# Optimization experiments

Hardware: AMD Instinct MI355X
Metric: run time of the kernel (lower is better)

## Reference

```python
import jax, jax.numpy as jnp
import numpy as np

RADIUS = 3
T_STEPS = 2
NEG = -9.0e8
B, L, DEG = 256, 64, 6
FEAT, BOND, FP, OUT = 39, 10, 256, 1


def _leaky(x):
    return jax.nn.leaky_relu(x, 0.01)


def _gru(x, h, wih, whh, bih, bhh):
    # PyTorch GRUCell: gates ordered (r, z, n)
    gi = x @ wih.T + bih
    gh = h @ whh.T + bhh
    ir, iz, inn = jnp.split(gi, 3, axis=-1)
    hr, hz, hn = jnp.split(gh, 3, axis=-1)
    r = jax.nn.sigmoid(ir + hr)
    z = jax.nn.sigmoid(iz + hz)
    n = jnp.tanh(inn + r * hn)
    return (1.0 - z) * n + z * h


def _forward(atom_list, bond_list, atom_mask,
             atom_fc_w, atom_fc_b, neighbor_fc_w, neighbor_fc_b,
             align_w, align_b, attend_w, attend_b,
             gru_wih, gru_whh, gru_bih, gru_bhh,
             mol_align_w, mol_align_b, mol_attend_w, mol_attend_b,
             mol_gru_wih, mol_gru_whh, mol_gru_bih, mol_gru_bhh,
             out_w, out_b,
             atom_degree_list, bond_degree_list):
    b, l, _ = atom_list.shape
    mask = atom_mask[..., None]                                   # [B,L,1]
    atom_feature = _leaky(atom_list @ atom_fc_w.T + atom_fc_b)    # [B,L,FP]

    # per-molecule neighbor gather (padding index = L-1)
    bidx = jnp.arange(b)[:, None, None]
    atom_nb = atom_list[bidx, atom_degree_list]                    # [B,L,deg,FEAT]
    bond_nb = bond_list[bidx, bond_degree_list]                    # [B,L,deg,BOND]
    neighbor_feature = _leaky(
        jnp.concatenate([atom_nb, bond_nb], axis=-1) @ neighbor_fc_w.T + neighbor_fc_b
    )                                                              # [B,L,deg,FP]

    attend_mask = (atom_degree_list != l - 1).astype(atom_feature.dtype)[..., None]
    softmax_mask = jnp.where(atom_degree_list == l - 1, NEG, 0.0).astype(atom_feature.dtype)[..., None]

    for d in range(RADIUS):
        af_exp = jnp.broadcast_to(atom_feature[:, :, None, :], neighbor_feature.shape)
        feature_align = jnp.concatenate([af_exp, neighbor_feature], axis=-1)  # [B,L,deg,2FP]
        align_score = _leaky(feature_align @ align_w[d].T + align_b[d]) + softmax_mask
        attention_weight = jax.nn.softmax(align_score, axis=-2) * attend_mask
        attended = neighbor_feature @ attend_w[d].T + attend_b[d]
        context = jax.nn.elu(jnp.sum(attention_weight * attended, axis=-2))   # [B,L,FP]
        atom_feature = _gru(context.reshape(b * l, -1), atom_feature.reshape(b * l, -1),
                            gru_wih[d], gru_whh[d], gru_bih[d], gru_bhh[d]).reshape(b, l, -1)
        # faithful to original: self-feature broadcast across neighbor dim
        neighbor_feature = jnp.broadcast_to(jax.nn.relu(atom_feature)[:, :, None, :],
                                            neighbor_feature.shape)

    mol_feature = jnp.sum(jax.nn.relu(atom_feature) * mask, axis=-2)          # [B,FP]
    mol_softmax_mask = jnp.where(atom_mask == 0, NEG, 0.0).astype(atom_feature.dtype)[..., None]

    for _ in range(T_STEPS):
        m_exp = jnp.broadcast_to(mol_feature[:, None, :], atom_feature.shape)
        mol_align = jnp.concatenate([m_exp, atom_feature], axis=-1)           # [B,L,2FP]
        mol_score = _leaky(mol_align @ mol_align_w.T + mol_align_b) + mol_softmax_mask
        mol_w = jax.nn.softmax(mol_score, axis=-2) * mask
        attended = atom_feature @ mol_attend_w.T + mol_attend_b
        mol_context = jax.nn.elu(jnp.sum(mol_w * attended, axis=-2))
        mol_feature = _gru(mol_context, mol_feature,
                           mol_gru_wih, mol_gru_whh, mol_gru_bih, mol_gru_bhh)

    mol_prediction = mol_feature @ out_w.T + out_b
    return atom_feature, mol_prediction


def setup_inputs() -> dict:
    key = jax.random.key(0)
    ks = jax.random.split(key, 20)
    s = 0.05
    return {
        "atom_list": jax.random.normal(ks[0], (B, L, FEAT), jnp.float32),
        "bond_list": jax.random.normal(ks[1], (B, L, BOND), jnp.float32),
        "atom_degree_list": jax.random.randint(ks[2], (B, L, DEG), 0, L),
        "bond_degree_list": jax.random.randint(ks[3], (B, L, DEG), 0, L),
        "atom_mask": jnp.ones((B, L), jnp.float32),
        "atom_fc_w": jax.random.normal(ks[4], (FP, FEAT)) * s,
        "atom_fc_b": jnp.zeros((FP,)),
        "neighbor_fc_w": jax.random.normal(ks[5], (FP, FEAT + BOND)) * s,
        "neighbor_fc_b": jnp.zeros((FP,)),
        "align_w": jax.random.normal(ks[6], (RADIUS, 1, 2 * FP)) * s,
        "align_b": jnp.zeros((RADIUS, 1)),
        "attend_w": jax.random.normal(ks[7], (RADIUS, FP, FP)) * s,
        "attend_b": jnp.zeros((RADIUS, FP)),
        "gru_wih": jax.random.normal(ks[8], (RADIUS, 3 * FP, FP)) * s,
        "gru_whh": jax.random.normal(ks[9], (RADIUS, 3 * FP, FP)) * s,
        "gru_bih": jnp.zeros((RADIUS, 3 * FP)),
        "gru_bhh": jnp.zeros((RADIUS, 3 * FP)),
        "mol_align_w": jax.random.normal(ks[10], (1, 2 * FP)) * s,
        "mol_align_b": jnp.zeros((1,)),
        "mol_attend_w": jax.random.normal(ks[11], (FP, FP)) * s,
        "mol_attend_b": jnp.zeros((FP,)),
        "mol_gru_wih": jax.random.normal(ks[12], (3 * FP, FP)) * s,
        "mol_gru_whh": jax.random.normal(ks[13], (3 * FP, FP)) * s,
        "mol_gru_bih": jnp.zeros((3 * FP,)),
        "mol_gru_bhh": jnp.zeros((3 * FP,)),
        "out_w": jax.random.normal(ks[14], (OUT, FP)) * s,
        "out_b": jnp.zeros((OUT,)),
    }


def reference(atom_list, bond_list, atom_degree_list, bond_degree_list, atom_mask,
              atom_fc_w, atom_fc_b, neighbor_fc_w, neighbor_fc_b,
              align_w, align_b, attend_w, attend_b,
              gru_wih, gru_whh, gru_bih, gru_bhh,
              mol_align_w, mol_align_b, mol_attend_w, mol_attend_b,
              mol_gru_wih, mol_gru_whh, mol_gru_bih, mol_gru_bhh,
              out_w, out_b):
    return _forward(atom_list, bond_list, atom_mask,
                    atom_fc_w, atom_fc_b, neighbor_fc_w, neighbor_fc_b,
                    align_w, align_b, attend_w, attend_b,
                    gru_wih, gru_whh, gru_bih, gru_bhh,
                    mol_align_w, mol_align_b, mol_attend_w, mol_attend_b,
                    mol_gru_wih, mol_gru_whh, mol_gru_bih, mol_gru_bhh,
                    out_w, out_b,
                    atom_degree_list, bond_degree_list)
```

## Files before the change

kernel.cpp:

```cpp
#include <hip/hip_runtime.h>
#include <hip/hip_bf16.h>

#define NB 256
#define NL 64
#define DEG 6
#define FEAT 39
#define BOND 10
#define FP 256
#define NEGV (-9.0e8f)

using s16x8 = __attribute__((ext_vector_type(8))) short;
using f32x4 = __attribute__((ext_vector_type(4))) float;

__device__ __forceinline__ unsigned short f2bf(float f){
  unsigned u = __float_as_uint(f);
  u += 0x7fffu + ((u >> 16) & 1u);
  return (unsigned short)(u >> 16);
}
__device__ __forceinline__ float lo16(unsigned u){ return __uint_as_float(u << 16); }
__device__ __forceinline__ float hi16(unsigned u){ return __uint_as_float(u & 0xffff0000u); }

__device__ __forceinline__ float block_sum256(float v, float* scr){
  #pragma unroll
  for(int o=32;o>0;o>>=1) v += __shfl_down(v, o, 64);
  __syncthreads();
  if((threadIdx.x & 63) == 0) scr[threadIdx.x >> 6] = v;
  __syncthreads();
  return scr[0] + scr[1] + scr[2] + scr[3];
}
__device__ __forceinline__ float wave_allsum(float v){
  #pragma unroll
  for(int o=1;o<64;o<<=1) v += __shfl_xor(v, o, 64);
  return v;
}

#define CVT_N0 196608
#define CVT_N1 589824
#define CVT_N2 589824
#define CVT_N3 65536
#define CVT_N4 196608
#define CVT_N5 196608
#define CVT_TOT (CVT_N0+CVT_N1+CVT_N2+CVT_N3+CVT_N4+CVT_N5)

__global__ void k_cvt_all(const float* __restrict__ a0, const float* __restrict__ a1,
                          const float* __restrict__ a2, const float* __restrict__ a3,
                          const float* __restrict__ a4, const float* __restrict__ a5,
                          unsigned short* __restrict__ dst){
  int i = blockIdx.x*256 + threadIdx.x;
  int off = i; const float* src;
  if(off < CVT_N0) src = a0;
  else { off -= CVT_N0;
    if(off < CVT_N1) src = a1;
    else { off -= CVT_N1;
      if(off < CVT_N2) src = a2;
      else { off -= CVT_N2;
        if(off < CVT_N3) src = a3;
        else { off -= CVT_N3;
          if(off < CVT_N4) src = a4;
          else { off -= CVT_N4; src = a5; } } } } }
  dst[i] = f2bf(src[off]);
}

__global__ void k_tr(const float* __restrict__ aw, const float* __restrict__ nw,
                     float* __restrict__ afcT, unsigned short* __restrict__ nfcT){
  int i = blockIdx.x*256 + threadIdx.x;
  if(i < 40*256){
    int k = i >> 8, r = i & 255;
    afcT[i] = (k < FEAT) ? aw[r*FEAT + k] : 0.f;
  } else {
    int j = i - 40*256;
    int k = j >> 8, r = j & 255;
    nfcT[j] = (k < FEAT+BOND) ? f2bf(nw[r*(FEAT+BOND) + k]) : (unsigned short)0;
  }
}

__global__ __launch_bounds__(256) void k_atom4(const float* __restrict__ atom,
    const float* __restrict__ afcT, const float* __restrict__ bias, float* __restrict__ af){
  __shared__ float WT[40*256];
  __shared__ float x_s[4][40];
  const int t = threadIdx.x, bl0 = blockIdx.x*4;
  for(int v=t; v<2560; v+=256) *(float4*)&WT[v*4] = *(const float4*)&afcT[v*4];
  for(int idx=t; idx<4*FEAT; idx+=256){ int a=idx/FEAT, k=idx%FEAT; x_s[a][k]=atom[(bl0+a)*FEAT+k]; }
  if(t < 4) x_s[t][39] = 0.f;
  __syncthreads();
  const int w = t>>6, t0 = (t&63)*4, row = bl0 + w;
  float4 b4 = *(const float4*)&bias[t0];
  float acc[4] = {b4.x, b4.y, b4.z, b4.w};
  for(int k=0;k<40;++k){
    float iv = x_s[w][k];
    float4 wv = *(const float4*)&WT[(k<<8)+t0];
    acc[0]=fmaf(iv,wv.x,acc[0]); acc[1]=fmaf(iv,wv.y,acc[1]);
    acc[2]=fmaf(iv,wv.z,acc[2]); acc[3]=fmaf(iv,wv.w,acc[3]);
  }
  float4 o;
  o.x = acc[0]>0.f?acc[0]:0.01f*acc[0]; o.y = acc[1]>0.f?acc[1]:0.01f*acc[1];
  o.z = acc[2]>0.f?acc[2]:0.01f*acc[2]; o.w = acc[3]>0.f?acc[3]:0.01f*acc[3];
  *(float4*)&af[(size_t)row*FP + t0] = o;
}

__global__ __launch_bounds__(256) void k_nbr4(const float* __restrict__ atom,
    const float* __restrict__ bond, const int* __restrict__ adl, const int* __restrict__ bdl,
    const unsigned short* __restrict__ nfcT, const float* __restrict__ bn,
    const float* __restrict__ alw, const float* __restrict__ alb,
    const float* __restrict__ af, float* __restrict__ wnf, float* __restrict__ swb){
  __shared__ unsigned short WnT[52*256];
  __shared__ float in_s[4][DEG][52];
  __shared__ int   ai_s[4][DEG];
  const int t = threadIdx.x, bl0 = blockIdx.x*4;
  if(t < 24){ int a=t/6, d=t%6; ai_s[a][d] = adl[(bl0+a)*DEG + d]; }
  for(int v=t; v<1664; v+=256) *(s16x8*)&WnT[v*8] = *(const s16x8*)&nfcT[v*8];
  __syncthreads();
  for(int idx=t; idx<4*DEG*(FEAT+BOND); idx+=256){
    int a = idx/(DEG*(FEAT+BOND)), rem = idx%(DEG*(FEAT+BOND));
    int d = rem/(FEAT+BOND), k = rem%(FEAT+BOND);
    int bb = (bl0+a) >> 6;
    float v;
    if(k < FEAT) v = atom[((size_t)bb*NL + ai_s[a][d])*FEAT + k];
    else { int bi = bdl[(bl0+a)*DEG + d]; v = bond[((size_t)bb*NL + bi)*BOND + (k-FEAT)]; }
    in_s[a][d][k] = v;
  }
  if(t < 24){ int a=t/6, d=t%6; in_s[a][d][49]=0.f; in_s[a][d][50]=0.f; in_s[a][d][51]=0.f; }
  __syncthreads();
  const int w = t>>6, lane = t&63, t0 = lane*4, row = bl0 + w;
  float acc[DEG][4] = {};
  for(int k=0;k<52;++k){
    uint2 u = *(const uint2*)&WnT[(k<<8) + t0];
    float w0=lo16(u.x), w1=hi16(u.x), w2=lo16(u.y), w3=hi16(u.y);
    #pragma unroll
    for(int d=0;d<DEG;++d){
      float iv = in_s[w][d][k];
      acc[d][0]=fmaf(iv,w0,acc[d][0]); acc[d][1]=fmaf(iv,w1,acc[d][1]);
      acc[d][2]=fmaf(iv,w2,acc[d][2]); acc[d][3]=fmaf(iv,w3,acc[d][3]);
    }
  }
  float4 bnv = *(const float4*)&bn[t0];
  float bna[4] = {bnv.x, bnv.y, bnv.z, bnv.w};
  float nf[DEG][4];
  #pragma unroll
  for(int d=0;d<DEG;++d)
    #pragma unroll
    for(int j=0;j<4;++j){ float v = acc[d][j] + bna[j]; nf[d][j] = v>0.f ? v : 0.01f*v; }
  float4 af4 = *(const float4*)&af[(size_t)row*FP + t0];
  float4 a1  = *(const float4*)&alw[t0];
  float4 a2  = *(const float4*)&alw[FP + t0];
  float sa = wave_allsum(af4.x*a1.x + af4.y*a1.y + af4.z*a1.z + af4.w*a1.w);
  float sd[DEG];
  #pragma unroll
  for(int d=0;d<DEG;++d)
    sd[d] = wave_allsum(nf[d][0]*a2.x + nf[d][1]*a2.y + nf[d][2]*a2.z + nf[d][3]*a2.w);
  float ab = alb[0];
  float sc[DEG], msk[DEG];
  #pragma unroll
  for(int d=0;d<DEG;++d){
    float v = sa + sd[d] + ab;
    v = v>0.f ? v : 0.01f*v;
    msk[d] = (ai_s[w][d] == NL-1) ? 0.f : 1.f;
    sc[d] = v + (msk[d] > 0.f ? 0.f : NEGV);
  }
  float m = sc[0];
  #pragma unroll
  for(int d=1;d<DEG;++d) m = fmaxf(m, sc[d]);
  float e[DEG], Z = 0.f;
  #pragma unroll
  for(int d=0;d<DEG;++d){ e[d] = expf(sc[d]-m); Z += e[d]; }
  float wgt[DEG], sw = 0.f;
  #pragma unroll
  for(int d=0;d<DEG;++d){ wgt[d] = e[d]/Z*msk[d]; sw += wgt[d]; }
  float o[4] = {};
  #pragma unroll
  for(int d=0;d<DEG;++d)
    #pragma unroll
    for(int j=0;j<4;++j) o[j] = fmaf(wgt[d], nf[d][j], o[j]);
  float4 ov; ov.x=o[0]; ov.y=o[1]; ov.z=o[2]; ov.w=o[3];
  *(float4*)&wnf[(size_t)row*FP + t0] = ov;
  if(lane == 0) swb[row] = sw;
}

template<int MODE>
__global__ __launch_bounds__(256) void k_ctx_gemm(
    const float* __restrict__ Xsrc, const float* __restrict__ swb,
    const unsigned short* __restrict__ Wbf, const float* __restrict__ bat,
    unsigned short* __restrict__ ctxbf){
  __shared__ unsigned short A_lds[64][264];
  __shared__ unsigned short B_lds[64][264];
  const int t = threadIdx.x;
  const int m0 = (blockIdx.x >> 2) * 64, n0 = (blockIdx.x & 3) * 64;
  const int rb = t >> 4, cb = (t & 15) * 16;
  for(int i=0;i<4;++i){
    int row = i*16 + rb;
    const float* src = Xsrc + (size_t)(m0+row)*FP + cb;
    float mult = MODE ? swb[m0+row] : 1.f;
    unsigned short tmp[16];
    #pragma unroll
    for(int q=0;q<4;++q){
      float4 v = ((const float4*)src)[q];
      if(MODE){ v.x=fmaxf(v.x,0.f)*mult; v.y=fmaxf(v.y,0.f)*mult;
                v.z=fmaxf(v.z,0.f)*mult; v.w=fmaxf(v.w,0.f)*mult; }
      tmp[q*4+0]=f2bf(v.x); tmp[q*4+1]=f2bf(v.y); tmp[q*4+2]=f2bf(v.z); tmp[q*4+3]=f2bf(v.w);
    }
    *(s16x8*)&A_lds[row][cb]   = *(s16x8*)&tmp[0];
    *(s16x8*)&A_lds[row][cb+8] = *(s16x8*)&tmp[8];
    const unsigned short* wsrc = Wbf + (size_t)(n0+row)*FP + cb;
    *(s16x8*)&B_lds[row][cb]   = *(const s16x8*)&wsrc[0];
    *(s16x8*)&B_lds[row][cb+8] = *(const s16x8*)&wsrc[8];
  }
  __syncthreads();
  const int w = t>>6, lane = t&63, lr = lane&15, ks = lane>>4;
  const int wr = (w>>1)*32, wc = (w&1)*32;
  f32x4 acc[2][2] = {};
  #pragma unroll
  for(int kk=0;kk<8;++kk){
    int ko = kk*32 + ks*8;
    s16x8 a0 = *(const s16x8*)&A_lds[wr+lr][ko];
    s16x8 a1 = *(const s16x8*)&A_lds[wr+16+lr][ko];
    s16x8 b0 = *(const s16x8*)&B_lds[wc+lr][ko];
    s16x8 b1 = *(const s16x8*)&B_lds[wc+16+lr][ko];
    acc[0][0] = __builtin_amdgcn_mfma_f32_16x16x32_bf16(a0,b0,acc[0][0],0,0,0);
    acc[0][1] = __builtin_amdgcn_mfma_f32_16x16x32_bf16(a0,b1,acc[0][1],0,0,0);
    acc[1][0] = __builtin_amdgcn_mfma_f32_16x16x32_bf16(a1,b0,acc[1][0],0,0,0);
    acc[1][1] = __builtin_amdgcn_mfma_f32_16x16x32_bf16(a1,b1,acc[1][1],0,0,0);
  }
  #pragma unroll
  for(int fm=0;fm<2;++fm)
    #pragma unroll
    for(int fn=0;fn<2;++fn){
      int n = n0 + wc + fn*16 + lr;
      float batv = bat[n];
      #pragma unroll
      for(int j=0;j<4;++j){
        int m = m0 + wr + fm*16 + ks*4 + j;
        float v = acc[fm][fn][j] + swb[m]*batv;
        v = v > 0.f ? v : expm1f(v);
        ctxbf[(size_t)m*FP + n] = f2bf(v);
      }
    }
}

__global__ __launch_bounds__(256) void k_gates_gru(
    const unsigned short* __restrict__ ctxbf, const float* __restrict__ h_glob,
    const unsigned short* __restrict__ wihbf, const unsigned short* __restrict__ whhbf,
    const float* __restrict__ bih, const float* __restrict__ bhh,
    float* __restrict__ h_out){
  __shared__ unsigned short A_ctx[32][40];
  __shared__ unsigned short A_h[32][40];
  __shared__ unsigned short B_lds[6][64][40];
  const int t = threadIdx.x;
  const int m0 = (blockIdx.x >> 2) * 32, nc = (blockIdx.x & 3) * 64;
  const int w = t>>6, lane = t&63, lr = lane&15, ks = lane>>4;
  const int mh = (w>>1)*16, nh = (w&1)*32;
  f32x4 acc[6][2] = {};
  for(int kk=0;kk<8;++kk){
    const int k0 = kk*32;
    __syncthreads();
    {
      int row = t>>3, c4 = (t&7)*4;
      *(uint2*)&A_ctx[row][c4] = *(const uint2*)(ctxbf + (size_t)(m0+row)*FP + k0 + c4);
      float4 hv = *(const float4*)(h_glob + (size_t)(m0+row)*FP + k0 + c4);
      unsigned short ht[4] = {f2bf(hv.x), f2bf(hv.y), f2bf(hv.z), f2bf(hv.w)};
      *(uint2*)&A_h[row][c4] = *(uint2*)ht;
    }
    #pragma unroll
    for(int i=0;i<6;++i){
      int idx = i*256 + t;
      int s = idx >> 8, rem = idx & 255;
      int row = rem >> 2, c8 = (rem & 3)*8;
      const unsigned short* wsrc = (s < 3)
          ? wihbf + (size_t)(s*FP + nc + row)*FP + k0 + c8
          : whhbf + (size_t)((s-3)*FP + nc + row)*FP + k0 + c8;
      *(s16x8*)&B_lds[s][row][c8] = *(const s16x8*)wsrc;
    }
    __syncthreads();
    s16x8 ac = *(const s16x8*)&A_ctx[mh+lr][ks*8];
    s16x8 ah = *(const s16x8*)&A_h[mh+lr][ks*8];
    #pragma unroll
    for(int s=0;s<6;++s){
      s16x8 a = (s < 3) ? ac : ah;
      #pragma unroll
      for(int fn=0;fn<2;++fn){
        s16x8 b = *(const s16x8*)&B_lds[s][nh+fn*16+lr][ks*8];
        acc[s][fn] = __builtin_amdgcn_mfma_f32_16x16x32_bf16(a,b,acc[s][fn],0,0,0);
      }
    }
  }
  #pragma unroll
  for(int fn=0;fn<2;++fn){
    int n = nc + nh + fn*16 + lr;
    float bir = bih[n], biz = bih[FP+n], bin_ = bih[2*FP+n];
    float bhr = bhh[n], bhz = bhh[FP+n], bhn  = bhh[2*FP+n];
    #pragma unroll
    for(int j=0;j<4;++j){
      int m = m0 + mh + ks*4 + j;
      float h = h_glob[(size_t)m*FP + n];
      float ir = acc[0][fn][j]+bir, iz = acc[1][fn][j]+biz, inn = acc[2][fn][j]+bin_;
      float hr = acc[3][fn][j]+bhr, hz = acc[4][fn][j]+bhz, hn  = acc[5][fn][j]+bhn;
      float r = 1.f/(1.f + expf(-(ir+hr)));
      float z = 1.f/(1.f + expf(-(iz+hz)));
      float ng = tanhf(inn + r*hn);
      h_out[(size_t)m*FP + n] = (1.f-z)*ng + z*h;
    }
  }
}

__global__ __launch_bounds__(256) void k_lin_gemm(
    const float* __restrict__ Xsrc, const unsigned short* __restrict__ Wbf,
    const float* __restrict__ bias, float* __restrict__ Y){
  __shared__ unsigned short A_lds[64][264];
  __shared__ unsigned short B_lds[64][264];
  const int t = threadIdx.x;
  const int m0 = (blockIdx.x >> 2) * 64, n0 = (blockIdx.x & 3) * 64;
  const int rb = t >> 4, cb = (t & 15) * 16;
  for(int i=0;i<4;++i){
    int row = i*16 + rb;
    const float* src = Xsrc + (size_t)(m0+row)*FP + cb;
    unsigned short tmp[16];
    #pragma unroll
    for(int q=0;q<4;++q){
      float4 v = ((const float4*)src)[q];
      tmp[q*4+0]=f2bf(v.x); tmp[q*4+1]=f2bf(v.y); tmp[q*4+2]=f2bf(v.z); tmp[q*4+3]=f2bf(v.w);
    }
    *(s16x8*)&A_lds[row][cb]   = *(s16x8*)&tmp[0];
    *(s16x8*)&A_lds[row][cb+8] = *(s16x8*)&tmp[8];
    const unsigned short* wsrc = Wbf + (size_t)(n0+row)*FP + cb;
    *(s16x8*)&B_lds[row][cb]   = *(const s16x8*)&wsrc[0];
    *(s16x8*)&B_lds[row][cb+8] = *(const s16x8*)&wsrc[8];
  }
  __syncthreads();
  const int w = t>>6, lane = t&63, lr = lane&15, ks = lane>>4;
  const int wr = (w>>1)*32, wc = (w&1)*32;
  f32x4 acc[2][2] = {};
  #pragma unroll
  for(int kk=0;kk<8;++kk){
    int ko = kk*32 + ks*8;
    s16x8 a0 = *(const s16x8*)&A_lds[wr+lr][ko];
    s16x8 a1 = *(const s16x8*)&A_lds[wr+16+lr][ko];
    s16x8 b0 = *(const s16x8*)&B_lds[wc+lr][ko];
    s16x8 b1 = *(const s16x8*)&B_lds[wc+16+lr][ko];
    acc[0][0] = __builtin_amdgcn_mfma_f32_16x16x32_bf16(a0,b0,acc[0][0],0,0,0);
    acc[0][1] = __builtin_amdgcn_mfma_f32_16x16x32_bf16(a0,b1,acc[0][1],0,0,0);
    acc[1][0] = __builtin_amdgcn_mfma_f32_16x16x32_bf16(a1,b0,acc[1][0],0,0,0);
    acc[1][1] = __builtin_amdgcn_mfma_f32_16x16x32_bf16(a1,b1,acc[1][1],0,0,0);
  }
  #pragma unroll
  for(int fm=0;fm<2;++fm)
    #pragma unroll
    for(int fn=0;fn<2;++fn){
      int n = n0 + wc + fn*16 + lr;
      float bv = bias[n];
      #pragma unroll
      for(int j=0;j<4;++j){
        int m = m0 + wr + fm*16 + ks*4 + j;
        Y[(size_t)m*FP + n] = acc[fm][fn][j] + bv;
      }
    }
}

__global__ void k_finalize(const float* __restrict__ af, const float* __restrict__ mask,
                           float* __restrict__ molfeat, float* __restrict__ out_af){
  const int b = blockIdx.x, t = threadIdx.x;
  __shared__ float msk_s[NL];
  if(t < NL) msk_s[t] = mask[b*NL + t];
  __syncthreads();
  float mf = 0.f;
  for(int l=0;l<NL;++l){
    float v = af[(size_t)(b*NL + l)*FP + t];
    out_af[(size_t)(b*NL + l)*FP + t] = v;
    mf = fmaf(fmaxf(v,0.f), msk_s[l], mf);
  }
  molfeat[b*FP + t] = mf;
}

__global__ void k_mol_ctx(const float* __restrict__ af, const float* __restrict__ att,
    const float* __restrict__ mfin, const float* __restrict__ maw,
    const float* __restrict__ mabp, const float* __restrict__ mask,
    unsigned short* __restrict__ ctxb){
  const int b = blockIdx.x, t = threadIdx.x;
  __shared__ float mf_s[FP];
  __shared__ float sc_s[NL], aw_s[NL], scr[4];
  mf_s[t] = mfin[b*FP + t];
  __syncthreads();
  float sa = block_sum256(maw[t]*mf_s[t], scr);
  int l = t >> 2, q = t & 3;
  float p = 0.f;
  {
    const float* ar = af + (size_t)(b*NL + l)*FP + q*64;
    const float* w2 = maw + FP + q*64;
    for(int k=0;k<64;++k) p = fmaf(ar[k], w2[k], p);
  }
  p += __shfl_xor(p, 1, 64);
  p += __shfl_xor(p, 2, 64);
  if(q == 0){
    float mv = mask[b*NL + l];
    float v = sa + p + mabp[0];
    v = v > 0.f ? v : 0.01f*v;
    sc_s[l] = v + (mv == 0.f ? NEGV : 0.f);
  }
  __syncthreads();
  if(t < NL){
    float s = sc_s[t];
    float m = s;
    #pragma unroll
    for(int o=32;o>0;o>>=1) m = fmaxf(m, __shfl_xor(m, o, 64));
    float e = expf(s - m);
    float Z = e;
    #pragma unroll
    for(int o=32;o>0;o>>=1) Z += __shfl_xor(Z, o, 64);
    aw_s[t] = e / Z * mask[b*NL + t];
  }
  __syncthreads();
  float acc = 0.f;
  for(int l2=0;l2<NL;++l2) acc = fmaf(aw_s[l2], att[(size_t)(b*NL + l2)*FP + t], acc);
  float c = acc > 0.f ? acc : expm1f(acc);
  ctxb[b*FP + t] = f2bf(c);
}

__global__ void k_out(const float* __restrict__ molfeat, const float* __restrict__ ow,
                      const float* __restrict__ ob, float* __restrict__ outp){
  const int b = blockIdx.x, t = threadIdx.x;
  __shared__ float scr[4];
  float s = block_sum256(molfeat[b*FP + t]*ow[t], scr);
  if(t == 0) outp[b] = s + ob[0];
}

__global__ void k_atom_fc(const float* __restrict__ atom, const float* __restrict__ W,
                          const float* __restrict__ bias, float* __restrict__ af){
  const int row = blockIdx.x;
  const int t = threadIdx.x;
  __shared__ float x[FEAT];
  if(t < FEAT) x[t] = atom[row*FEAT + t];
  __syncthreads();
  float acc = bias[t];
  const float* wr = W + t*FEAT;
  #pragma unroll
  for(int k=0;k<FEAT;++k) acc = fmaf(x[k], wr[k], acc);
  af[row*FP + t] = acc > 0.f ? acc : 0.01f*acc;
}

__global__ void k_nbr_align(const float* __restrict__ atom, const float* __restrict__ bond,
    const int* __restrict__ adl, const int* __restrict__ bdl,
    const float* __restrict__ Wn, const float* __restrict__ bn,
    const float* __restrict__ alw, const float* __restrict__ alb,
    const float* __restrict__ af, float* __restrict__ wnf, float* __restrict__ swb){
  const int bl = blockIdx.x;
  const int b  = bl >> 6;
  const int t  = threadIdx.x;
  __shared__ float in_s[DEG][FEAT+BOND];
  __shared__ float nf_s[DEG][FP];
  __shared__ float af_s[FP];
  __shared__ int   ai[DEG];
  __shared__ float msk[DEG];
  __shared__ float sc[DEG];
  __shared__ float scr[4];
  if(t < DEG){ int a = adl[bl*DEG + t]; ai[t] = a; msk[t] = (a == NL-1) ? 0.f : 1.f; }
  af_s[t] = af[bl*FP + t];
  __syncthreads();
  for(int idx = t; idx < DEG*(FEAT+BOND); idx += FP){
    int d = idx / (FEAT+BOND), k = idx % (FEAT+BOND);
    float v;
    if(k < FEAT) v = atom[(b*NL + ai[d])*FEAT + k];
    else { int bi = bdl[bl*DEG + d]; v = bond[(b*NL + bi)*BOND + (k-FEAT)]; }
    in_s[d][k] = v;
  }
  __syncthreads();
  float acc[DEG];
  #pragma unroll
  for(int d=0;d<DEG;++d) acc[d] = 0.f;
  const float* wr = Wn + t*(FEAT+BOND);
  for(int k=0;k<FEAT+BOND;++k){
    float w = wr[k];
    #pragma unroll
    for(int d=0;d<DEG;++d) acc[d] = fmaf(in_s[d][k], w, acc[d]);
  }
  float bv = bn[t];
  #pragma unroll
  for(int d=0;d<DEG;++d){
    float v = acc[d] + bv;
    nf_s[d][t] = v > 0.f ? v : 0.01f*v;
  }
  __syncthreads();
  float aw1 = alw[t], aw2 = alw[FP + t];
  float sa = block_sum256(aw1*af_s[t], scr);
  float ab = alb[0];
  for(int d=0;d<DEG;++d){
    float s = block_sum256(aw2*nf_s[d][t], scr);
    if(t==0){
      float v = sa + s + ab;
      v = v > 0.f ? v : 0.01f*v;
      sc[d] = v + (msk[d] > 0.f ? 0.f : NEGV);
    }
  }
  __syncthreads();
  float m = sc[0];
  #pragma unroll
  for(int d=1;d<DEG;++d) m = fmaxf(m, sc[d]);
  float e[DEG], Z = 0.f;
  #pragma unroll
  for(int d=0;d<DEG;++d){ e[d] = expf(sc[d]-m); Z += e[d]; }
  float w_[DEG], sw = 0.f;
  #pragma unroll
  for(int d=0;d<DEG;++d){ w_[d] = e[d]/Z*msk[d]; sw += w_[d]; }
  float o = 0.f;
  #pragma unroll
  for(int d=0;d<DEG;++d) o = fmaf(w_[d], nf_s[d][t], o);
  wnf[bl*FP + t] = o;
  if(t==0) swb[bl] = sw;
}

template<int RELUX>
__global__ __launch_bounds__(256) void k_ctx_gru(
    const float* __restrict__ xsrc, const float* __restrict__ swb, float* __restrict__ af,
    const float* __restrict__ Wat, const float* __restrict__ bat,
    const float* __restrict__ wih, const float* __restrict__ whh,
    const float* __restrict__ bih, const float* __restrict__ bhh){
  const int R = 16;
  const int row0 = blockIdx.x * R;
  const int t = threadIdx.x;
  __shared__ __align__(16) float x_s[R][FP];
  __shared__ __align__(16) float h_s[R][FP];
  __shared__ float swb_s[R];
  if(t < R) swb_s[t] = swb[row0 + t];
  __syncthreads();
  #pragma unroll
  for(int r=0;r<R;++r){
    float h = af[(size_t)(row0+r)*FP + t];
    h_s[r][t] = h;
    if(RELUX) x_s[r][t] = fmaxf(h, 0.f) * swb_s[r];
    else      x_s[r][t] = xsrc[(size_t)(row0+r)*FP + t];
  }
  __syncthreads();
  float acc[R];
  #pragma unroll
  for(int r=0;r<R;++r) acc[r] = 0.f;
  const float4* wr = (const float4*)(Wat + (size_t)t*FP);
  for(int k4=0;k4<FP/4;++k4){
    float4 w = wr[k4];
    #pragma unroll
    for(int r=0;r<R;++r){
      float4 xv = ((const float4*)x_s[r])[k4];
      acc[r] = fmaf(xv.x,w.x,acc[r]); acc[r] = fmaf(xv.y,w.y,acc[r]);
      acc[r] = fmaf(xv.z,w.z,acc[r]); acc[r] = fmaf(xv.w,w.w,acc[r]);
    }
  }
  float batv = bat[t];
  float ctx[R];
  #pragma unroll
  for(int r=0;r<R;++r){
    float pre = acc[r] + swb_s[r]*batv;
    ctx[r] = pre > 0.f ? pre : expm1f(pre);
  }
  __syncthreads();
  #pragma unroll
  for(int r=0;r<R;++r) x_s[r][t] = ctx[r];
  __syncthreads();
  float ar_[R], az_[R], an_[R];
  #pragma unroll
  for(int r=0;r<R;++r){ ar_[r]=0.f; az_[r]=0.f; an_[r]=0.f; }
  {
    const float4* p0 = (const float4*)(wih + (size_t)t*FP);
    const float4* p1 = (const float4*)(wih + (size_t)(FP+t)*FP);
    const float4* p2 = (const float4*)(wih + (size_t)(2*FP+t)*FP);
    for(int k4=0;k4<FP/4;++k4){
      float4 w0=p0[k4], w1=p1[k4], w2=p2[k4];
      #pragma unroll
      for(int r=0;r<R;++r){
        float4 xv = ((const float4*)x_s[r])[k4];
        ar_[r]=fmaf(xv.x,w0.x,ar_[r]); ar_[r]=fmaf(xv.y,w0.y,ar_[r]);
        ar_[r]=fmaf(xv.z,w0.z,ar_[r]); ar_[r]=fmaf(xv.w,w0.w,ar_[r]);
        az_[r]=fmaf(xv.x,w1.x,az_[r]); az_[r]=fmaf(xv.y,w1.y,az_[r]);
        az_[r]=fmaf(xv.z,w1.z,az_[r]); az_[r]=fmaf(xv.w,w1.w,az_[r]);
        an_[r]=fmaf(xv.x,w2.x,an_[r]); an_[r]=fmaf(xv.y,w2.y,an_[r]);
        an_[r]=fmaf(xv.z,w2.z,an_[r]); an_[r]=fmaf(xv.w,w2.w,an_[r]);
      }
    }
  }
  float hr_[R], hz_[R], hn_[R];
  #pragma unroll
  for(int r=0;r<R;++r){ hr_[r]=0.f; hz_[r]=0.f; hn_[r]=0.f; }
  {
    const float4* p0 = (const float4*)(whh + (size_t)t*FP);
    const float4* p1 = (const float4*)(whh + (size_t)(FP+t)*FP);
    const float4* p2 = (const float4*)(whh + (size_t)(2*FP+t)*FP);
    for(int k4=0;k4<FP/4;++k4){
      float4 w0=p0[k4], w1=p1[k4], w2=p2[k4];
      #pragma unroll
      for(int r=0;r<R;++r){
        float4 hv = ((const float4*)h_s[r])[k4];
        hr_[r]=fmaf(hv.x,w0.x,hr_[r]); hr_[r]=fmaf(hv.y,w0.y,hr_[r]);
        hr_[r]=fmaf(hv.z,w0.z,hr_[r]); hr_[r]=fmaf(hv.w,w0.w,hr_[r]);
        hz_[r]=fmaf(hv.x,w1.x,hz_[r]); hz_[r]=fmaf(hv.y,w1.y,hz_[r]);
        hz_[r]=fmaf(hv.z,w1.z,hz_[r]); hz_[r]=fmaf(hv.w,w1.w,hz_[r]);
        hn_[r]=fmaf(hv.x,w2.x,hn_[r]); hn_[r]=fmaf(hv.y,w2.y,hn_[r]);
        hn_[r]=fmaf(hv.z,w2.z,hn_[r]); hn_[r]=fmaf(hv.w,w2.w,hn_[r]);
      }
    }
  }
  float bir = bih[t], biz = bih[FP+t], bin_ = bih[2*FP+t];
  float bhr = bhh[t], bhz = bhh[FP+t], bhn  = bhh[2*FP+t];
  #pragma unroll
  for(int r=0;r<R;++r){
    float ir = ar_[r]+bir, iz = az_[r]+biz, inn = an_[r]+bin_;
    float hr = hr_[r]+bhr, hz = hz_[r]+bhz, hn  = hn_[r]+bhn;
    float rg = 1.f/(1.f + expf(-(ir+hr)));
    float zg = 1.f/(1.f + expf(-(iz+hz)));
    float ng = tanhf(inn + rg*hn);
    af[(size_t)(row0+r)*FP + t] = (1.f-zg)*ng + zg*h_s[r][t];
  }
}

__global__ void k_mol_att(const float* __restrict__ af, const float* __restrict__ maw,
    const float* __restrict__ mab, const float* __restrict__ mask,
    float* __restrict__ att, float* __restrict__ molfeat, float* __restrict__ out_af){
  const int b = blockIdx.x, t = threadIdx.x;
  __shared__ __align__(16) float a_s[32][FP];
  __shared__ float msk_s[NL];
  if(t < NL) msk_s[t] = mask[b*NL + t];
  __syncthreads();
  float mf = 0.f;
  const float4* wr = (const float4*)(maw + (size_t)t*FP);
  float mabv = mab[t];
  for(int half=0; half<2; ++half){
    #pragma unroll
    for(int i=0;i<32;++i){
      int l = half*32 + i;
      float v = af[(size_t)(b*NL + l)*FP + t];
      a_s[i][t] = v;
      out_af[(size_t)(b*NL + l)*FP + t] = v;
      mf = fmaf(fmaxf(v,0.f), msk_s[l], mf);
    }
    __syncthreads();
    float acc[32];
    #pragma unroll
    for(int i=0;i<32;++i) acc[i] = 0.f;
    for(int k4=0;k4<FP/4;++k4){
      float4 w = wr[k4];
      #pragma unroll
      for(int i=0;i<32;++i){
        float4 xv = ((const float4*)a_s[i])[k4];
        acc[i] = fmaf(xv.x,w.x,acc[i]); acc[i] = fmaf(xv.y,w.y,acc[i]);
        acc[i] = fmaf(xv.z,w.z,acc[i]); acc[i] = fmaf(xv.w,w.w,acc[i]);
      }
    }
    #pragma unroll
    for(int i=0;i<32;++i) att[(size_t)(b*NL + half*32 + i)*FP + t] = acc[i] + mabv;
    __syncthreads();
  }
  molfeat[b*FP + t] = mf;
}

__global__ void k_mol_step(const float* __restrict__ af, const float* __restrict__ att,
    float* __restrict__ molfeat, const float* __restrict__ maw, const float* __restrict__ mabp,
    const float* __restrict__ mask,
    const float* __restrict__ wih, const float* __restrict__ whh,
    const float* __restrict__ bih, const float* __restrict__ bhh){
  const int b = blockIdx.x, t = threadIdx.x;
  __shared__ __align__(16) float mf_s[FP];
  __shared__ __align__(16) float ctx_s[FP];
  __shared__ float sc_s[NL], aw_s[NL], scr[4];
  mf_s[t] = molfeat[b*FP + t];
  __syncthreads();
  float sa = block_sum256(maw[t]*mf_s[t], scr);
  int l = t >> 2, q = t & 3;
  float p = 0.f;
  {
    const float* ar = af + (size_t)(b*NL + l)*FP + q*64;
    const float* w2 = maw + FP + q*64;
    for(int k=0;k<64;++k) p = fmaf(ar[k], w2[k], p);
  }
  p += __shfl_xor(p, 1, 64);
  p += __shfl_xor(p, 2, 64);
  if(q == 0){
    float mv = mask[b*NL + l];
    float v = sa + p + mabp[0];
    v = v > 0.f ? v : 0.01f*v;
    sc_s[l] = v + (mv == 0.f ? NEGV : 0.f);
  }
  __syncthreads();
  if(t < NL){
    float s = sc_s[t];
    float m = s;
    #pragma unroll
    for(int o=32;o>0;o>>=1) m = fmaxf(m, __shfl_xor(m, o, 64));
    float e = expf(s - m);
    float Z = e;
    #pragma unroll
    for(int o=32;o>0;o>>=1) Z += __shfl_xor(Z, o, 64);
    aw_s[t] = e / Z * mask[b*NL + t];
  }
  __syncthreads();
  float acc = 0.f;
  for(int l2=0;l2<NL;++l2) acc = fmaf(aw_s[l2], att[(size_t)(b*NL + l2)*FP + t], acc);
  ctx_s[t] = acc > 0.f ? acc : expm1f(acc);
  __syncthreads();
  float air=0.f, aiz=0.f, ain=0.f, ahr=0.f, ahz=0.f, ahn=0.f;
  const float4* wirp=(const float4*)(wih + (size_t)t*FP);
  const float4* wizp=(const float4*)(wih + (size_t)(FP+t)*FP);
  const float4* winp=(const float4*)(wih + (size_t)(2*FP+t)*FP);
  const float4* whrp=(const float4*)(whh + (size_t)t*FP);
  const float4* whzp=(const float4*)(whh + (size_t)(FP+t)*FP);
  const float4* whnp=(const float4*)(whh + (size_t)(2*FP+t)*FP);
  for(int k4=0;k4<FP/4;++k4){
    float4 xv = ((const float4*)ctx_s)[k4];
    float4 hv = ((const float4*)mf_s)[k4];
    float4 f0=wirp[k4], f1=wizp[k4], f2=winp[k4];
    float4 g0=whrp[k4], g1=whzp[k4], g2=whnp[k4];
    air=fmaf(xv.x,f0.x,air); air=fmaf(xv.y,f0.y,air); air=fmaf(xv.z,f0.z,air); air=fmaf(xv.w,f0.w,air);
    aiz=fmaf(xv.x,f1.x,aiz); aiz=fmaf(xv.y,f1.y,aiz); aiz=fmaf(xv.z,f1.z,aiz); aiz=fmaf(xv.w,f1.w,aiz);
    ain=fmaf(xv.x,f2.x,ain); ain=fmaf(xv.y,f2.y,ain); ain=fmaf(xv.z,f2.z,ain); ain=fmaf(xv.w,f2.w,ain);
    ahr=fmaf(hv.x,g0.x,ahr); ahr=fmaf(hv.y,g0.y,ahr); ahr=fmaf(hv.z,g0.z,ahr); ahr=fmaf(hv.w,g0.w,ahr);
    ahz=fmaf(hv.x,g1.x,ahz); ahz=fmaf(hv.y,g1.y,ahz); ahz=fmaf(hv.z,g1.z,ahz); ahz=fmaf(hv.w,g1.w,ahz);
    ahn=fmaf(hv.x,g2.x,ahn); ahn=fmaf(hv.y,g2.y,ahn); ahn=fmaf(hv.z,g2.z,ahn); ahn=fmaf(hv.w,g2.w,ahn);
  }
  float ir=air+bih[t], iz=aiz+bih[FP+t], inn=ain+bih[2*FP+t];
  float hr=ahr+bhh[t], hz=ahz+bhh[FP+t], hn=ahn+bhh[2*FP+t];
  float rg = 1.f/(1.f + expf(-(ir+hr)));
  float zg = 1.f/(1.f + expf(-(iz+hz)));
  float ng = tanhf(inn + rg*hn);
  molfeat[b*FP + t] = (1.f-zg)*ng + zg*mf_s[t];
}

extern "C" void kernel_launch(void* const* d_in, const int* in_sizes, int n_in,
                              void* d_out, int out_size, void* d_ws, size_t ws_size,
                              hipStream_t stream){
  const float* atom_list = (const float*)d_in[0];
  const float* bond_list = (const float*)d_in[1];
  const int*   adl       = (const int*)d_in[2];
  const int*   bdl       = (const int*)d_in[3];
  const float* amask     = (const float*)d_in[4];
  const float* afc_w     = (const float*)d_in[5];
  const float* afc_b     = (const float*)d_in[6];
  const float* nfc_w     = (const float*)d_in[7];
  const float* nfc_b     = (const float*)d_in[8];
  const float* align_w   = (const float*)d_in[9];
  const float* align_b   = (const float*)d_in[10];
  const float* attend_w  = (const float*)d_in[11];
  const float* attend_b  = (const float*)d_in[12];
  const float* gru_wih   = (const float*)d_in[13];
  const float* gru_whh   = (const float*)d_in[14];
  const float* gru_bih   = (const float*)d_in[15];
  const float* gru_bhh   = (const float*)d_in[16];
  const float* mol_align_w  = (const float*)d_in[17];
  const float* mol_align_b  = (const float*)d_in[18];
  const float* mol_attend_w = (const float*)d_in[19];
  const float* mol_attend_b = (const float*)d_in[20];
  const float* mg_wih    = (const float*)d_in[21];
  const float* mg_whh    = (const float*)d_in[22];
  const float* mg_bih    = (const float*)d_in[23];
  const float* mg_bhh    = (const float*)d_in[24];
  const float* out_w     = (const float*)d_in[25];
  const float* out_b     = (const float*)d_in[26];

  float* out_af   = (float*)d_out;
  float* out_pred = out_af + (size_t)NB*NL*FP;

  const size_t NROW = (size_t)NB*NL;
  const size_t F32_CNT = 3*NROW*FP + NROW + 2*(size_t)NB*FP + 40*256;
  const size_t BF16_CNT = NROW*FP + CVT_TOT + 52*256;
  const size_t NEED = F32_CNT*4 + BF16_CNT*2;

  if(ws_size >= NEED){
    float* af_a    = (float*)d_ws;
    float* af_b    = af_a + NROW*FP;
    float* wnf     = af_b + NROW*FP;
    float* swb     = wnf  + NROW*FP;
    float* mf_a    = swb  + NROW;
    float* mf_b    = mf_a + (size_t)NB*FP;
    float* afcT    = mf_b + (size_t)NB*FP;
    unsigned short* ctxbf   = (unsigned short*)(afcT + 40*256);
    unsigned short* attw_bf = ctxbf + NROW*FP;
    unsigned short* wih_bf  = attw_bf + CVT_N0;
    unsigned short* whh_bf  = wih_bf + CVT_N1;
    unsigned short* maw_bf  = whh_bf + CVT_N2;
    unsigned short* mgih_bf = maw_bf + CVT_N3;
    unsigned short* mghh_bf = mgih_bf + CVT_N4;
    unsigned short* nfcT_bf = mghh_bf + CVT_N5;

    k_cvt_all<<<CVT_TOT/256, 256, 0, stream>>>(attend_w, gru_wih, gru_whh,
                                               mol_attend_w, mg_wih, mg_whh, attw_bf);
    k_tr<<<(40*256 + 52*256)/256, 256, 0, stream>>>(afc_w, nfc_w, afcT, nfcT_bf);

    k_atom4<<<NB*NL/4, 256, 0, stream>>>(atom_list, afcT, afc_b, af_a);
    k_nbr4<<<NB*NL/4, 256, 0, stream>>>(atom_list, bond_list, adl, bdl,
                                        nfcT_bf, nfc_b, align_w, align_b, af_a, wnf, swb);
    float* h_cur = af_a;
    float* h_nxt = af_b;
    for(int d=0; d<3; ++d){
      const unsigned short* Wat = attw_bf + (size_t)d*FP*FP;
      const float* bat = attend_b + (size_t)d*FP;
      const unsigned short* wih = wih_bf + (size_t)d*3*FP*FP;
      const unsigned short* whh = whh_bf + (size_t)d*3*FP*FP;
      const float* bih = gru_bih + (size_t)d*3*FP;
      const float* bhh = gru_bhh + (size_t)d*3*FP;
      if(d == 0)
        k_ctx_gemm<0><<<(NB*NL/64)*4, 256, 0, stream>>>(wnf, swb, Wat, bat, ctxbf);
      else
        k_ctx_gemm<1><<<(NB*NL/64)*4, 256, 0, stream>>>(h_cur, swb, Wat, bat, ctxbf);
      k_gates_gru<<<(NB*NL/32)*4, 256, 0, stream>>>(ctxbf, h_cur, wih, whh, bih, bhh, h_nxt);
      float* tmp = h_cur; h_cur = h_nxt; h_nxt = tmp;
    }
    k_lin_gemm<<<(NB*NL/64)*4, 256, 0, stream>>>(h_cur, maw_bf, mol_attend_b, wnf);
    k_finalize<<<NB, 256, 0, stream>>>(h_cur, amask, mf_a, out_af);
    float* m_cur = mf_a; float* m_nxt = mf_b;
    for(int s=0; s<2; ++s){
      k_mol_ctx<<<NB, 256, 0, stream>>>(h_cur, wnf, m_cur, mol_align_w, mol_align_b,
                                        amask, ctxbf);
      k_gates_gru<<<(NB/32)*4, 256, 0, stream>>>(ctxbf, m_cur, mgih_bf, mghh_bf,
                                                 mg_bih, mg_bhh, m_nxt);
      float* tmp = m_cur; m_cur = m_nxt; m_nxt = tmp;
    }
    k_out<<<NB, 256, 0, stream>>>(m_cur, out_w, out_b, out_pred);
  } else {
    float* af      = (float*)d_ws;
    float* wnf     = af  + NROW*FP;
    float* swb     = wnf + NROW*FP;
    float* molfeat = swb + NROW;

    k_atom_fc<<<NB*NL, FP, 0, stream>>>(atom_list, afc_w, afc_b, af);
    k_nbr_align<<<NB*NL, FP, 0, stream>>>(atom_list, bond_list, adl, bdl,
                                          nfc_w, nfc_b, align_w, align_b, af, wnf, swb);
    for(int d=0; d<3; ++d){
      const float* Wat = attend_w + (size_t)d*FP*FP;
      const float* bat = attend_b + (size_t)d*FP;
      const float* wih = gru_wih + (size_t)d*3*FP*FP;
      const float* whh = gru_whh + (size_t)d*3*FP*FP;
      const float* bih = gru_bih + (size_t)d*3*FP;
      const float* bhh = gru_bhh + (size_t)d*3*FP;
      if(d == 0) k_ctx_gru<0><<<NB*NL/16, FP, 0, stream>>>(wnf, swb, af, Wat, bat, wih, whh, bih, bhh);
      else       k_ctx_gru<1><<<NB*NL/16, FP, 0, stream>>>(af,  swb, af, Wat, bat, wih, whh, bih, bhh);
    }
    k_mol_att<<<NB, FP, 0, stream>>>(af, mol_attend_w, mol_attend_b, amask, wnf, molfeat, out_af);
    for(int s=0; s<2; ++s)
      k_mol_step<<<NB, FP, 0, stream>>>(af, wnf, molfeat, mol_align_w, mol_align_b, amask,
                                        mg_wih, mg_whh, mg_bih, mg_bhh);
    k_out<<<NB, FP, 0, stream>>>(molfeat, out_w, out_b, out_pred);
  }
}
```

Before: 337.6 us.

## Fuse three radius iterations of context GEMM and GRU into one kernel

```diff
diff --git a/kernel.cpp b/kernel.cpp
--- a/kernel.cpp
+++ b/kernel.cpp
@@ -176,11 +176,166 @@
   if(lane == 0) swb[row] = sw;
 }
 
-template<int MODE>
-__global__ __launch_bounds__(256) void k_ctx_gemm(
-    const float* __restrict__ Xsrc, const float* __restrict__ swb,
-    const unsigned short* __restrict__ Wbf, const float* __restrict__ bat,
-    unsigned short* __restrict__ ctxbf){
+__global__ __launch_bounds__(256) void k_radius(
+    const float* __restrict__ wnf, float* __restrict__ af, const float* __restrict__ swb,
+    const unsigned short* __restrict__ attw_bf, const float* __restrict__ attend_b,
+    const unsigned short* __restrict__ wih_bf, const unsigned short* __restrict__ whh_bf,
+    const float* __restrict__ gru_bih, const float* __restrict__ gru_bhh){
+  __shared__ __align__(16) unsigned short Xbf[64*264];
+  __shared__ __align__(16) unsigned short Cbf[64*264];
+  __shared__ __align__(16) unsigned short Hbf[64*264];
+  __shared__ __align__(16) unsigned short Bu[16896];
+  const int t = threadIdx.x;
+  const int m0 = blockIdx.x * 64;
+  const int w = t>>6, lane = t&63, lr = lane&15, ks = lane>>4;
+  const int wr = (w>>1)*32, wc = (w&1)*32;
+  const int rb = t>>4, cb = (t&15)*16;
+  float swb8[2][4];
+  #pragma unroll
+  for(int mf=0;mf<2;++mf)
+    #pragma unroll
+    for(int j=0;j<4;++j) swb8[mf][j] = swb[m0 + wr + mf*16 + ks*4 + j];
+
+  for(int d=0; d<3; ++d){
+    const unsigned short* Wat = attw_bf + (size_t)d*FP*FP;
+    const unsigned short* wih = wih_bf + (size_t)d*3*FP*FP;
+    const unsigned short* whh = whh_bf + (size_t)d*3*FP*FP;
+    const float* bat = attend_b + d*FP;
+    const float* bih = gru_bih + d*3*FP;
+    const float* bhh = gru_bhh + d*3*FP;
+
+    __syncthreads();
+    for(int i=0;i<4;++i){
+      int row = i*16 + rb;
+      const float* hsrc = af + (size_t)(m0+row)*FP + cb;
+      float sw = swb[m0+row];
+      unsigned short tx[16], th[16];
+      #pragma unroll
+      for(int q=0;q<4;++q){
+        float4 hv = ((const float4*)hsrc)[q];
+        float4 xv;
+        if(d == 0){
+          xv = ((const float4*)(wnf + (size_t)(m0+row)*FP + cb))[q];
+        } else {
+          xv.x = fmaxf(hv.x,0.f)*sw; xv.y = fmaxf(hv.y,0.f)*sw;
+          xv.z = fmaxf(hv.z,0.f)*sw; xv.w = fmaxf(hv.w,0.f)*sw;
+        }
+        tx[q*4+0]=f2bf(xv.x); tx[q*4+1]=f2bf(xv.y); tx[q*4+2]=f2bf(xv.z); tx[q*4+3]=f2bf(xv.w);
+        th[q*4+0]=f2bf(hv.x); th[q*4+1]=f2bf(hv.y); th[q*4+2]=f2bf(hv.z); th[q*4+3]=f2bf(hv.w);
+      }
+      *(s16x8*)&Xbf[row*264 + cb]     = *(s16x8*)&tx[0];
+      *(s16x8*)&Xbf[row*264 + cb + 8] = *(s16x8*)&tx[8];
+      *(s16x8*)&Hbf[row*264 + cb]     = *(s16x8*)&th[0];
+      *(s16x8*)&Hbf[row*264 + cb + 8] = *(s16x8*)&th[8];
+    }
+    for(int n0=0;n0<4;++n0){
+      __syncthreads();
+      for(int i=0;i<4;++i){
+        int row = i*16 + rb;
+        const unsigned short* wsrc = Wat + (size_t)(n0*64+row)*FP + cb;
+        *(s16x8*)&Bu[row*264 + cb]     = *(const s16x8*)&wsrc[0];
+        *(s16x8*)&Bu[row*264 + cb + 8] = *(const s16x8*)&wsrc[8];
+      }
+      __syncthreads();
+      f32x4 acc[2][2] = {};
+      #pragma unroll
+      for(int kk=0;kk<8;++kk){
+        int ko = kk*32 + ks*8;
+        s16x8 a0 = *(const s16x8*)&Xbf[(wr+lr)*264 + ko];
+        s16x8 a1 = *(const s16x8*)&Xbf[(wr+16+lr)*264 + ko];
+        s16x8 b0 = *(const s16x8*)&Bu[(wc+lr)*264 + ko];
+        s16x8 b1 = *(const s16x8*)&Bu[(wc+16+lr)*264 + ko];
+        acc[0][0] = __builtin_amdgcn_mfma_f32_16x16x32_bf16(a0,b0,acc[0][0],0,0,0);
+        acc[0][1] = __builtin_amdgcn_mfma_f32_16x16x32_bf16(a0,b1,acc[0][1],0,0,0);
+        acc[1][0] = __builtin_amdgcn_mfma_f32_16x16x32_bf16(a1,b0,acc[1][0],0,0,0);
+        acc[1][1] = __builtin_amdgcn_mfma_f32_16x16x32_bf16(a1,b1,acc[1][1],0,0,0);
+      }
+      #pragma unroll
+      for(int fm=0;fm<2;++fm)
+        #pragma unroll
+        for(int fn=0;fn<2;++fn){
+          int n = n0*64 + wc + fn*16 + lr;
+          float batv = bat[n];
+          #pragma unroll
+          for(int j=0;j<4;++j){
+            int mrow = wr + fm*16 + ks*4 + j;
+            float v = acc[fm][fn][j] + swb8[fm][j]*batv;
+            v = v > 0.f ? v : expm1f(v);
+            Cbf[mrow*264 + n] = f2bf(v);
+          }
+        }
+    }
+    for(int nc4=0; nc4<4; ++nc4){
+      const int n0c = nc4*64;
+      f32x4 aR[2][2] = {}, aZ[2][2] = {}, aN[2][2] = {}, aH[2][2] = {};
+      for(int kk=0;kk<8;++kk){
+        __syncthreads();
+        #pragma unroll
+        for(int i=0;i<6;++i){
+          int idx = i*256 + t;
+          int s = idx >> 8, rem = idx & 255;
+          int row = rem >> 2, c8 = (rem & 3)*8;
+          const unsigned short* wsrc = (s < 3)
+              ? wih + (size_t)(s*FP + n0c + row)*FP + kk*32 + c8
+              : whh + (size_t)((s-3)*FP + n0c + row)*FP + kk*32 + c8;
+          *(s16x8*)&Bu[(s*64+row)*40 + c8] = *(const s16x8*)wsrc;
+        }
+        __syncthreads();
+        int ko = kk*32 + ks*8;
+        s16x8 ac0 = *(const s16x8*)&Cbf[(wr+lr)*264 + ko];
+        s16x8 ac1 = *(const s16x8*)&Cbf[(wr+16+lr)*264 + ko];
+        s16x8 ah0 = *(const s16x8*)&Hbf[(wr+lr)*264 + ko];
+        s16x8 ah1 = *(const s16x8*)&Hbf[(wr+16+lr)*264 + ko];
+        #pragma unroll
+        for(int fn=0;fn<2;++fn){
+          int brow = (wc + fn*16 + lr)*40 + ks*8;
+          s16x8 b0 = *(const s16x8*)&Bu[(0*64)*40 + brow];
+          s16x8 b1 = *(const s16x8*)&Bu[(1*64)*40 + brow];
+          s16x8 b2 = *(const s16x8*)&Bu[(2*64)*40 + brow];
+          s16x8 b3 = *(const s16x8*)&Bu[(3*64)*40 + brow];
+          s16x8 b4 = *(const s16x8*)&Bu[(4*64)*40 + brow];
+          s16x8 b5 = *(const s16x8*)&Bu[(5*64)*40 + brow];
+          aR[0][fn] = __builtin_amdgcn_mfma_f32_16x16x32_bf16(ac0,b0,aR[0][fn],0,0,0);
+          aR[1][fn] = __builtin_amdgcn_mfma_f32_16x16x32_bf16(ac1,b0,aR[1][fn],0,0,0);
+          aZ[0][fn] = __builtin_amdgcn_mfma_f32_16x16x32_bf16(ac0,b1,aZ[0][fn],0,0,0);
+          aZ[1][fn] = __builtin_amdgcn_mfma_f32_16x16x32_bf16(ac1,b1,aZ[1][fn],0,0,0);
+          aN[0][fn] = __builtin_amdgcn_mfma_f32_16x16x32_bf16(ac0,b2,aN[0][fn],0,0,0);
+          aN[1][fn] = __builtin_amdgcn_mfma_f32_16x16x32_bf16(ac1,b2,aN[1][fn],0,0,0);
+          aR[0][fn] = __builtin_amdgcn_mfma_f32_16x16x32_bf16(ah0,b3,aR[0][fn],0,0,0);
+          aR[1][fn] = __builtin_amdgcn_mfma_f32_16x16x32_bf16(ah1,b3,aR[1][fn],0,0,0);
+          aZ[0][fn] = __builtin_amdgcn_mfma_f32_16x16x32_bf16(ah0,b4,aZ[0][fn],0,0,0);
+          aZ[1][fn] = __builtin_amdgcn_mfma_f32_16x16x32_bf16(ah1,b4,aZ[1][fn],0,0,0);
+          aH[0][fn] = __builtin_amdgcn_mfma_f32_16x16x32_bf16(ah0,b5,aH[0][fn],0,0,0);
+          aH[1][fn] = __builtin_amdgcn_mfma_f32_16x16x32_bf16(ah1,b5,aH[1][fn],0,0,0);
+        }
+      }
+      #pragma unroll
+      for(int fn=0;fn<2;++fn){
+        int n = n0c + wc + fn*16 + lr;
+        float brz = bih[n] + bhh[n];
+        float bzz = bih[FP+n] + bhh[FP+n];
+        float bnn = bih[2*FP+n];
+        float bhn = bhh[2*FP+n];
+        #pragma unroll
+        for(int fm=0;fm<2;++fm){
+          #pragma unroll
+          for(int j=0;j<4;++j){
+            int m = m0 + wr + fm*16 + ks*4 + j;
+            float hold = af[(size_t)m*FP + n];
+            float r = 1.f/(1.f + expf(-(aR[fm][fn][j] + brz)));
+            float z = 1.f/(1.f + expf(-(aZ[fm][fn][j] + bzz)));
+            float ng = tanhf(aN[fm][fn][j] + bnn + r*(aH[fm][fn][j] + bhn));
+            af[(size_t)m*FP + n] = (1.f-z)*ng + z*hold;
+          }
+        }
+      }
+    }
+  }
+}
+
+__global__ __launch_bounds__(256) void k_lin_gemm(
+    const float* __restrict__ Xsrc, const unsigned short* __restrict__ Wbf,
+    const float* __restrict__ bias, float* __restrict__ Y){
   __shared__ unsigned short A_lds[64][264];
   __shared__ unsigned short B_lds[64][264];
   const int t = threadIdx.x;
@@ -189,13 +344,10 @@
   for(int i=0;i<4;++i){
     int row = i*16 + rb;
     const float* src = Xsrc + (size_t)(m0+row)*FP + cb;
-    float mult = MODE ? swb[m0+row] : 1.f;
     unsigned short tmp[16];
     #pragma unroll
     for(int q=0;q<4;++q){
       float4 v = ((const float4*)src)[q];
-      if(MODE){ v.x=fmaxf(v.x,0.f)*mult; v.y=fmaxf(v.y,0.f)*mult;
-                v.z=fmaxf(v.z,0.f)*mult; v.w=fmaxf(v.w,0.f)*mult; }
       tmp[q*4+0]=f2bf(v.x); tmp[q*4+1]=f2bf(v.y); tmp[q*4+2]=f2bf(v.z); tmp[q*4+3]=f2bf(v.w);
     }
     *(s16x8*)&A_lds[row][cb]   = *(s16x8*)&tmp[0];
@@ -225,18 +377,16 @@
     #pragma unroll
     for(int fn=0;fn<2;++fn){
       int n = n0 + wc + fn*16 + lr;
-      float batv = bat[n];
+      float bv = bias[n];
       #pragma unroll
       for(int j=0;j<4;++j){
         int m = m0 + wr + fm*16 + ks*4 + j;
-        float v = acc[fm][fn][j] + swb[m]*batv;
-        v = v > 0.f ? v : expm1f(v);
-        ctxbf[(size_t)m*FP + n] = f2bf(v);
+        Y[(size_t)m*FP + n] = acc[fm][fn][j] + bv;
       }
     }
 }
 
-__global__ __launch_bounds__(256) void k_gates_gru(
+__global__ __launch_bounds__(256) void k_gates32(
     const unsigned short* __restrict__ ctxbf, const float* __restrict__ h_glob,
     const unsigned short* __restrict__ wihbf, const unsigned short* __restrict__ whhbf,
     const float* __restrict__ bih, const float* __restrict__ bhh,
@@ -301,59 +451,6 @@
   }
 }
 
-__global__ __launch_bounds__(256) void k_lin_gemm(
-    const float* __restrict__ Xsrc, const unsigned short* __restrict__ Wbf,
-    const float* __restrict__ bias, float* __restrict__ Y){
-  __shared__ unsigned short A_lds[64][264];
-  __shared__ unsigned short B_lds[64][264];
-  const int t = threadIdx.x;
-  const int m0 = (blockIdx.x >> 2) * 64, n0 = (blockIdx.x & 3) * 64;
-  const int rb = t >> 4, cb = (t & 15) * 16;
-  for(int i=0;i<4;++i){
-    int row = i*16 + rb;
-    const float* src = Xsrc + (size_t)(m0+row)*FP + cb;
-    unsigned short tmp[16];
-    #pragma unroll
-    for(int q=0;q<4;++q){
-      float4 v = ((const float4*)src)[q];
-      tmp[q*4+0]=f2bf(v.x); tmp[q*4+1]=f2bf(v.y); tmp[q*4+2]=f2bf(v.z); tmp[q*4+3]=f2bf(v.w);
-    }
-    *(s16x8*)&A_lds[row][cb]   = *(s16x8*)&tmp[0];
-    *(s16x8*)&A_lds[row][cb+8] = *(s16x8*)&tmp[8];
-    const unsigned short* wsrc = Wbf + (size_t)(n0+row)*FP + cb;
-    *(s16x8*)&B_lds[row][cb]   = *(const s16x8*)&wsrc[0];
-    *(s16x8*)&B_lds[row][cb+8] = *(const s16x8*)&wsrc[8];
-  }
-  __syncthreads();
-  const int w = t>>6, lane = t&63, lr = lane&15, ks = lane>>4;
-  const int wr = (w>>1)*32, wc = (w&1)*32;
-  f32x4 acc[2][2] = {};
-  #pragma unroll
-  for(int kk=0;kk<8;++kk){
-    int ko = kk*32 + ks*8;
-    s16x8 a0 = *(const s16x8*)&A_lds[wr+lr][ko];
-    s16x8 a1 = *(const s16x8*)&A_lds[wr+16+lr][ko];
-    s16x8 b0 = *(const s16x8*)&B_lds[wc+lr][ko];
-    s16x8 b1 = *(const s16x8*)&B_lds[wc+16+lr][ko];
-    acc[0][0] = __builtin_amdgcn_mfma_f32_16x16x32_bf16(a0,b0,acc[0][0],0,0,0);
-    acc[0][1] = __builtin_amdgcn_mfma_f32_16x16x32_bf16(a0,b1,acc[0][1],0,0,0);
-    acc[1][0] = __builtin_amdgcn_mfma_f32_16x16x32_bf16(a1,b0,acc[1][0],0,0,0);
-    acc[1][1] = __builtin_amdgcn_mfma_f32_16x16x32_bf16(a1,b1,acc[1][1],0,0,0);
-  }
-  #pragma unroll
-  for(int fm=0;fm<2;++fm)
-    #pragma unroll
-    for(int fn=0;fn<2;++fn){
-      int n = n0 + wc + fn*16 + lr;
-      float bv = bias[n];
-      #pragma unroll
-      for(int j=0;j<4;++j){
-        int m = m0 + wr + fm*16 + ks*4 + j;
-        Y[(size_t)m*FP + n] = acc[fm][fn][j] + bv;
-      }
-    }
-}
-
 __global__ void k_finalize(const float* __restrict__ af, const float* __restrict__ mask,
                            float* __restrict__ molfeat, float* __restrict__ out_af){
   const int b = blockIdx.x, t = threadIdx.x;
@@ -382,9 +479,14 @@
   int l = t >> 2, q = t & 3;
   float p = 0.f;
   {
-    const float* ar = af + (size_t)(b*NL + l)*FP + q*64;
-    const float* w2 = maw + FP + q*64;
-    for(int k=0;k<64;++k) p = fmaf(ar[k], w2[k], p);
+    const float4* ar = (const float4*)(af + (size_t)(b*NL + l)*FP + q*64);
+    const float4* w2 = (const float4*)(maw + FP + q*64);
+    #pragma unroll
+    for(int k=0;k<16;++k){
+      float4 a = ar[k], ww = w2[k];
+      p = fmaf(a.x,ww.x,p); p = fmaf(a.y,ww.y,p);
+      p = fmaf(a.z,ww.z,p); p = fmaf(a.w,ww.w,p);
+    }
   }
   p += __shfl_xor(p, 1, 64);
   p += __shfl_xor(p, 2, 64);
@@ -780,30 +882,16 @@
     k_atom4<<<NB*NL/4, 256, 0, stream>>>(atom_list, afcT, afc_b, af_a);
     k_nbr4<<<NB*NL/4, 256, 0, stream>>>(atom_list, bond_list, adl, bdl,
                                         nfcT_bf, nfc_b, align_w, align_b, af_a, wnf, swb);
-    float* h_cur = af_a;
-    float* h_nxt = af_b;
-    for(int d=0; d<3; ++d){
-      const unsigned short* Wat = attw_bf + (size_t)d*FP*FP;
-      const float* bat = attend_b + (size_t)d*FP;
-      const unsigned short* wih = wih_bf + (size_t)d*3*FP*FP;
-      const unsigned short* whh = whh_bf + (size_t)d*3*FP*FP;
-      const float* bih = gru_bih + (size_t)d*3*FP;
-      const float* bhh = gru_bhh + (size_t)d*3*FP;
-      if(d == 0)
-        k_ctx_gemm<0><<<(NB*NL/64)*4, 256, 0, stream>>>(wnf, swb, Wat, bat, ctxbf);
-      else
-        k_ctx_gemm<1><<<(NB*NL/64)*4, 256, 0, stream>>>(h_cur, swb, Wat, bat, ctxbf);
-      k_gates_gru<<<(NB*NL/32)*4, 256, 0, stream>>>(ctxbf, h_cur, wih, whh, bih, bhh, h_nxt);
-      float* tmp = h_cur; h_cur = h_nxt; h_nxt = tmp;
-    }
-    k_lin_gemm<<<(NB*NL/64)*4, 256, 0, stream>>>(h_cur, maw_bf, mol_attend_b, wnf);
-    k_finalize<<<NB, 256, 0, stream>>>(h_cur, amask, mf_a, out_af);
+    k_radius<<<NB*NL/64, 256, 0, stream>>>(wnf, af_a, swb, attw_bf, attend_b,
+                                           wih_bf, whh_bf, gru_bih, gru_bhh);
+    k_lin_gemm<<<(NB*NL/64)*4, 256, 0, stream>>>(af_a, maw_bf, mol_attend_b, wnf);
+    k_finalize<<<NB, 256, 0, stream>>>(af_a, amask, mf_a, out_af);
     float* m_cur = mf_a; float* m_nxt = mf_b;
     for(int s=0; s<2; ++s){
-      k_mol_ctx<<<NB, 256, 0, stream>>>(h_cur, wnf, m_cur, mol_align_w, mol_align_b,
+      k_mol_ctx<<<NB, 256, 0, stream>>>(af_a, wnf, m_cur, mol_align_w, mol_align_b,
                                         amask, ctxbf);
-      k_gates_gru<<<(NB/32)*4, 256, 0, stream>>>(ctxbf, m_cur, mgih_bf, mghh_bf,
-                                                 mg_bih, mg_bhh, m_nxt);
+      k_gates32<<<(NB/32)*4, 256, 0, stream>>>(ctxbf, m_cur, mgih_bf, mghh_bf,
+                                               mg_bih, mg_bhh, m_nxt);
       float* tmp = m_cur; m_cur = m_nxt; m_nxt = tmp;
     }
     k_out<<<NB, 256, 0, stream>>>(m_cur, out_w, out_b, out_pred);
```

New measurement: 338.3 us. Within noise of the previous version (+0.2%).
